# Optimization experiments

Measured on AMD Instinct MI355X. Metric: run time of the kernel, lower is better.

The kernel has to match this reference:

```python
import jax, jax.numpy as jnp
import numpy as np

N = 100000
IN_CH = 1024
Z = 32
E = 1600000


def _gcn_conv(x, src, dst, W, b, n_nodes):
    # PyG GCNConv: add self-loops, symmetric deg^{-1/2} normalization,
    # message = norm * (x @ W)[src], scatter-add into dst, plus bias.
    loop = jnp.arange(n_nodes)
    s = jnp.concatenate([src, loop])
    d = jnp.concatenate([dst, loop])
    deg = jax.ops.segment_sum(jnp.ones_like(s, dtype=x.dtype), d, num_segments=n_nodes)
    dinv = jnp.where(deg > 0, jax.lax.rsqrt(deg), 0.0)
    norm = dinv[s] * dinv[d]                     # [E+N]
    h = x @ W                                    # [N, out]
    msg = h[s] * norm[:, None]                   # [E+N, out]
    out = jax.ops.segment_sum(msg, d, num_segments=n_nodes)
    return out + b


def setup_inputs() -> dict:
    key = jax.random.key(0)
    ks = jax.random.split(key, 10)
    x = jax.random.normal(ks[0], (N, IN_CH), dtype=jnp.float32)
    edge_index = jax.random.randint(ks[1], (2, E), 0, N, dtype=jnp.int64)
    def lin(k, fan_in, fan_out):
        bound = 1.0 / np.sqrt(fan_in)
        kw, kb = jax.random.split(k)
        W = jax.random.uniform(kw, (fan_in, fan_out), jnp.float32, -bound, bound)
        b = jax.random.uniform(kb, (fan_out,), jnp.float32, -bound, bound)
        return W, b
    Wg1, bg1 = lin(ks[2], IN_CH, 2 * Z)
    Wg2, bg2 = lin(ks[3], 2 * Z, Z)
    Wf1, bf1 = lin(ks[4], Z, 2 * Z)
    Wf2, bf2 = lin(ks[5], 2 * Z, IN_CH)
    return {"x": x, "edge_index": edge_index,
            "Wg1": Wg1, "bg1": bg1, "Wg2": Wg2, "bg2": bg2,
            "Wf1": Wf1, "bf1": bf1, "Wf2": Wf2, "bf2": bf2}


def reference(x, edge_index, Wg1, bg1, Wg2, bg2, Wf1, bf1, Wf2, bf2):
    src, dst = edge_index[0], edge_index[1]
    h = jax.nn.relu(_gcn_conv(x, src, dst, Wg1, bg1, N))
    z = _gcn_conv(h, src, dst, Wg2, bg2, N)          # encode output
    d = jax.nn.relu(z @ Wf1 + bf1)
    out = jax.nn.relu(d @ Wf2 + bf2)                 # decode output
    return out
```

## Files before the change

### kernel.cpp

```cpp
#include <hip/hip_runtime.h>

#define NN 100000
#define EE 1600000

using bf16x8 = __attribute__((ext_vector_type(8))) short;
using f32x4  = __attribute__((ext_vector_type(4))) float;

static __device__ __forceinline__ unsigned short f2bh(float f) {
    unsigned int u = __float_as_uint(f);
    return (unsigned short)((u + 0x7FFFu + ((u >> 16) & 1u)) >> 16);
}
static __device__ __forceinline__ float bh2f(unsigned short h) {
    return __uint_as_float(((unsigned int)h) << 16);
}

static __device__ __forceinline__ void split_pack(float4 a, float4 b,
                                                  bf16x8& h, bf16x8& l) {
    float f[8] = {a.x, a.y, a.z, a.w, b.x, b.y, b.z, b.w};
    union { bf16x8 v; unsigned int u[4]; } H, L;
    #pragma unroll
    for (int e = 0; e < 4; ++e) {
        unsigned int u0 = __float_as_uint(f[2 * e]);
        unsigned int u1 = __float_as_uint(f[2 * e + 1]);
        H.u[e] = (u0 >> 16) | (u1 & 0xFFFF0000u);
        float r0 = f[2 * e]     - __uint_as_float(u0 & 0xFFFF0000u);
        float r1 = f[2 * e + 1] - __uint_as_float(u1 & 0xFFFF0000u);
        L.u[e] = (__float_as_uint(r0) >> 16) | (__float_as_uint(r1) & 0xFFFF0000u);
    }
    h = H.v; l = L.v;
}

__global__ __launch_bounds__(256) void k_init(unsigned int* cursor) {
    int v = blockIdx.x * 256 + threadIdx.x;
    if (v < NN) cursor[v] = 0u;
}

__global__ __launch_bounds__(256) void k_fill(const int* __restrict__ src,
        const int* __restrict__ dst, unsigned int* cursor, int* __restrict__ bkt) {
    int e = blockIdx.x * 256 + threadIdx.x;
    if (e < EE) {
        int d = dst[e];
        unsigned int pos = atomicAdd(&cursor[d], 1u);
        bkt[(size_t)d * 64 + pos] = src[e];
    }
}

__global__ __launch_bounds__(256) void k_dinv(const unsigned int* __restrict__ deg, float* dinv) {
    int v = blockIdx.x * 256 + threadIdx.x;
    if (v < NN) dinv[v] = rsqrtf((float)(deg[v] + 1u));
}

__global__ __launch_bounds__(256) void k_prepW1(const float* __restrict__ W,
        unsigned short* __restrict__ img) {
    int t = blockIdx.x * 256 + threadIdx.x;
    int k = t >> 6, c = t & 63;
    float f = W[k * 64 + c];
    unsigned short h = f2bh(f);
    int chunk = k >> 5, kk = k & 31;
    size_t base = (size_t)chunk * 4608 + (size_t)c * 36 + kk;
    img[base] = h;
    img[base + 2304] = f2bh(f - bh2f(h));
}

__global__ __launch_bounds__(256) void k_prepW2(const float* __restrict__ W,
        unsigned short* __restrict__ wh, unsigned short* __restrict__ wl) {
    int t = blockIdx.x * 256 + threadIdx.x;
    int k = t >> 10, c = t & 1023;
    float f = W[k * 1024 + c];
    unsigned short h = f2bh(f);
    wh[c * 64 + k] = h;
    wl[c * 64 + k] = f2bh(f - bh2f(h));
}

__global__ __launch_bounds__(256) void k_gemm1(const float* __restrict__ x,
        const unsigned short* __restrict__ wimg,
        const float* __restrict__ dinv, float* __restrict__ g1) {
    __shared__ __align__(16) unsigned short bs[2][2][64][36];
    const int tid = threadIdx.x;
    const int lane = tid & 63, w = tid >> 6;
    const int l16 = lane & 15, g = lane >> 4;
    const int row0 = blockIdx.x * 64;
    const int rA = row0 + w * 16 + l16;
    const bool okA = rA < NN;
    const float* xp = x + (size_t)rA * 1024 + g * 8;
    const char* wb = (const char*)wimg;
    f32x4 acc[4] = {};
    for (int j = w; j < 9; j += 4)
        __builtin_amdgcn_global_load_lds((const unsigned int*)(wb + j * 1024 + lane * 16),
                                         (unsigned int*)((char*)&bs[0][0][0][0] + j * 1024), 16, 0, 0);
    float4 xr0 = make_float4(0.f,0.f,0.f,0.f), xr1 = xr0;
    if (okA) { xr0 = *(const float4*)(xp); xr1 = *(const float4*)(xp + 4); }
    __syncthreads();
    int cur = 0;
    for (int t = 0; t < 32; ++t) {
        float4 nx0 = make_float4(0.f,0.f,0.f,0.f), nx1 = nx0;
        if (t < 31) {
            const char* gb = wb + (size_t)(t + 1) * 9216;
            char* lb = (char*)&bs[cur ^ 1][0][0][0];
            for (int j = w; j < 9; j += 4)
                __builtin_amdgcn_global_load_lds((const unsigned int*)(gb + j * 1024 + lane * 16),
                                                 (unsigned int*)(lb + j * 1024), 16, 0, 0);
            if (okA) { nx0 = *(const float4*)(xp + (t + 1) * 32);
                       nx1 = *(const float4*)(xp + (t + 1) * 32 + 4); }
        }
        bf16x8 ah, al;
        split_pack(xr0, xr1, ah, al);
        #pragma unroll
        for (int nf = 0; nf < 4; ++nf) {
            bf16x8 bh = *(const bf16x8*)&bs[cur][0][nf * 16 + l16][g * 8];
            bf16x8 bl = *(const bf16x8*)&bs[cur][1][nf * 16 + l16][g * 8];
            acc[nf] = __builtin_amdgcn_mfma_f32_16x16x32_bf16(ah, bh, acc[nf], 0, 0, 0);
            acc[nf] = __builtin_amdgcn_mfma_f32_16x16x32_bf16(al, bh, acc[nf], 0, 0, 0);
            acc[nf] = __builtin_amdgcn_mfma_f32_16x16x32_bf16(ah, bl, acc[nf], 0, 0, 0);
        }
        __syncthreads();
        xr0 = nx0; xr1 = nx1; cur ^= 1;
    }
    #pragma unroll
    for (int r = 0; r < 4; ++r) {
        int node = row0 + w * 16 + g * 4 + r;
        if (node < NN) {
            float di = dinv[node];
            #pragma unroll
            for (int nf = 0; nf < 4; ++nf)
                g1[(size_t)node * 64 + nf * 16 + l16] = acc[nf][r] * di;
        }
    }
}

__global__ __launch_bounds__(256) void k_gather64(const float* __restrict__ g1,
        const int* __restrict__ bkt, const unsigned int* __restrict__ deg,
        const float* __restrict__ dinv, const float* __restrict__ bg1,
        float* __restrict__ h) {
    int wv = (blockIdx.x * 256 + threadIdx.x) >> 6;
    int lane = threadIdx.x & 63;
    if (wv >= NN) return;
    unsigned int n = deg[wv];
    const int* b = bkt + (size_t)wv * 64;
    float sum = g1[(size_t)wv * 64 + lane];
    unsigned int i = 0;
    for (; i + 4 <= n; i += 4) {
        int s0 = b[i], s1 = b[i + 1], s2 = b[i + 2], s3 = b[i + 3];
        float v0 = g1[(size_t)s0 * 64 + lane];
        float v1 = g1[(size_t)s1 * 64 + lane];
        float v2 = g1[(size_t)s2 * 64 + lane];
        float v3 = g1[(size_t)s3 * 64 + lane];
        sum += (v0 + v1) + (v2 + v3);
    }
    for (; i < n; ++i) sum += g1[(size_t)b[i] * 64 + lane];
    h[(size_t)wv * 64 + lane] = fmaxf(sum * dinv[wv] + bg1[lane], 0.f);
}

__global__ __launch_bounds__(256) void k_layer2(const float* __restrict__ h,
        const float* __restrict__ Wg2, const float* __restrict__ dinv,
        float* __restrict__ g2) {
    __shared__ __align__(16) float as[64][68];
    __shared__ __align__(16) float wsh[64][32];
    const int tid = threadIdx.x;
    const int node0 = blockIdx.x * 64;
    {
        const int lr = tid >> 4, lk = (tid & 15) * 4;
        #pragma unroll
        for (int l = 0; l < 4; ++l) {
            int r = lr + l * 16, v = node0 + r;
            float4 a = make_float4(0.f, 0.f, 0.f, 0.f);
            if (v < NN) a = *(const float4*)(h + (size_t)v * 64 + lk);
            *(float4*)&as[r][lk] = a;
        }
        const int wr = tid >> 3, wk = (tid & 7) * 4;
        #pragma unroll
        for (int l = 0; l < 2; ++l) {
            int r = wr + l * 32;
            *(float4*)&wsh[r][wk] = *(const float4*)(Wg2 + (size_t)r * 32 + wk);
        }
    }
    __syncthreads();
    const int tx = tid & 7, ty = tid >> 3;
    float acc[2][4] = {{0.f}};
    for (int kk = 0; kk < 64; kk += 4) {
        float wv[4][4];
        #pragma unroll
        for (int j = 0; j < 4; ++j)
            *(float4*)&wv[j][0] = *(const float4*)&wsh[kk + j][tx * 4];
        #pragma unroll
        for (int i = 0; i < 2; ++i) {
            float xv[4];
            *(float4*)&xv[0] = *(const float4*)&as[ty * 2 + i][kk];
            #pragma unroll
            for (int j = 0; j < 4; ++j) {
                #pragma unroll
                for (int c = 0; c < 4; ++c)
                    acc[i][c] += xv[j] * wv[j][c];
            }
        }
    }
    #pragma unroll
    for (int i = 0; i < 2; ++i) {
        int v = node0 + ty * 2 + i;
        if (v < NN) {
            float di = dinv[v];
            float4 o;
            o.x = acc[i][0] * di; o.y = acc[i][1] * di;
            o.z = acc[i][2] * di; o.w = acc[i][3] * di;
            *(float4*)(g2 + (size_t)v * 32 + tx * 4) = o;
        }
    }
}

__global__ __launch_bounds__(256) void k_gather32(const float* __restrict__ g2,
        const int* __restrict__ bkt, const unsigned int* __restrict__ deg,
        const float* __restrict__ dinv, const float* __restrict__ bg2,
        float* __restrict__ z) {
    int node = (blockIdx.x * 256 + threadIdx.x) >> 5;
    int c = threadIdx.x & 31;
    if (node >= NN) return;
    unsigned int n = deg[node];
    const int* b = bkt + (size_t)node * 64;
    float sum = g2[(size_t)node * 32 + c];
    unsigned int i = 0;
    for (; i + 4 <= n; i += 4) {
        int s0 = b[i], s1 = b[i + 1], s2 = b[i + 2], s3 = b[i + 3];
        float v0 = g2[(size_t)s0 * 32 + c];
        float v1 = g2[(size_t)s1 * 32 + c];
        float v2 = g2[(size_t)s2 * 32 + c];
        float v3 = g2[(size_t)s3 * 32 + c];
        sum += (v0 + v1) + (v2 + v3);
    }
    for (; i < n; ++i) sum += g2[(size_t)b[i] * 32 + c];
    z[(size_t)node * 32 + c] = sum * dinv[node] + bg2[c];
}

__global__ __launch_bounds__(256) void k_decode(const float* __restrict__ z,
        const float* __restrict__ Wf1, const float* __restrict__ bf1,
        const unsigned short* __restrict__ w2hg, const unsigned short* __restrict__ w2lg,
        const float* __restrict__ bf2, float* __restrict__ out) {
    __shared__ __align__(16) unsigned char smem[35328];
    float (*dsh)[68] = (float (*)[68])smem;
    float (*zs)[36]  = (float (*)[36])(smem + 17408);
    float (*w1s)[64] = (float (*)[64])(smem + 26624);
    unsigned short (*w2h)[72] = (unsigned short (*)[72])smem;
    unsigned short (*w2l)[72] = (unsigned short (*)[72])(smem + 9216);
    float (*ost)[66] = (float (*)[66])(smem + 18432);
    const int tid = threadIdx.x;
    const int lane = tid & 63, w = tid >> 6;
    const int l16 = lane & 15, g = lane >> 4;
    const int node0 = blockIdx.x * 64;

    uint4 ph[2], pl[2];
    #pragma unroll
    for (int j = 0; j < 2; ++j) {
        int fi = tid + 256 * j;
        int c = fi >> 3, k8 = (fi & 7) * 8;
        ph[j] = *(const uint4*)(w2hg + (size_t)c * 64 + k8);
        pl[j] = *(const uint4*)(w2lg + (size_t)c * 64 + k8);
    }

    #pragma unroll
    for (int j = 0; j < 2; ++j) {
        int fi = tid + 256 * j;
        int v = fi >> 3, m4 = (fi & 7) * 4;
        float4 zz = make_float4(0.f, 0.f, 0.f, 0.f);
        if (node0 + v < NN) zz = *(const float4*)(z + (size_t)(node0 + v) * 32 + m4);
        *(float4*)&zs[v][m4] = zz;
    }
    #pragma unroll
    for (int j = 0; j < 2; ++j) {
        int fi = tid + 256 * j;
        int r = fi >> 4, c4 = (fi & 15) * 4;
        *(float4*)&w1s[r][c4] = *(const float4*)(Wf1 + (size_t)r * 64 + c4);
    }
    __syncthreads();

    {
        const int dtx = tid & 15, dty = tid >> 4;
        float acc[4][4] = {{0.f}};
        for (int m = 0; m < 32; m += 4) {
            float wv[4][4];
            #pragma unroll
            for (int j = 0; j < 4; ++j)
                *(float4*)&wv[j][0] = *(const float4*)&w1s[m + j][dtx * 4];
            #pragma unroll
            for (int i = 0; i < 4; ++i) {
                float zv[4];
                *(float4*)&zv[0] = *(const float4*)&zs[dty * 4 + i][m];
                #pragma unroll
                for (int j = 0; j < 4; ++j) {
                    #pragma unroll
                    for (int c = 0; c < 4; ++c)
                        acc[i][c] += zv[j] * wv[j][c];
                }
            }
        }
        float4 b4 = *(const float4*)(bf1 + dtx * 4);
        #pragma unroll
        for (int i = 0; i < 4; ++i) {
            float4 dd;
            dd.x = fmaxf(acc[i][0] + b4.x, 0.f);
            dd.y = fmaxf(acc[i][1] + b4.y, 0.f);
            dd.z = fmaxf(acc[i][2] + b4.z, 0.f);
            dd.w = fmaxf(acc[i][3] + b4.w, 0.f);
            *(float4*)&dsh[dty * 4 + i][dtx * 4] = dd;
        }
    }
    __syncthreads();

    bf16x8 ah[2], al[2];
    {
        int row = w * 16 + l16;
        #pragma unroll
        for (int s = 0; s < 2; ++s) {
            int k0 = s * 32 + g * 8;
            float4 f0 = *(float4*)&dsh[row][k0];
            float4 f1 = *(float4*)&dsh[row][k0 + 4];
            float fv[8] = {f0.x, f0.y, f0.z, f0.w, f1.x, f1.y, f1.z, f1.w};
            bf16x8 hv, lv;
            #pragma unroll
            for (int e = 0; e < 8; ++e) {
                unsigned short hh = f2bh(fv[e]);
                hv[e] = (short)hh;
                lv[e] = (short)f2bh(fv[e] - bh2f(hh));
            }
            ah[s] = hv; al[s] = lv;
        }
    }
    __syncthreads();

    #pragma unroll
    for (int j = 0; j < 2; ++j) {
        int fi = tid + 256 * j;
        int c = fi >> 3, k8 = (fi & 7) * 8;
        *(uint4*)&w2h[c][k8] = ph[j];
        *(uint4*)&w2l[c][k8] = pl[j];
        ph[j] = *(const uint4*)(w2hg + (size_t)(64 + c) * 64 + k8);
        pl[j] = *(const uint4*)(w2lg + (size_t)(64 + c) * 64 + k8);
    }
    __syncthreads();

    for (int ch = 0; ch < 16; ++ch) {
        const int col0 = ch * 64;
        f32x4 acc[4] = {};
        #pragma unroll
        for (int nf = 0; nf < 4; ++nf) {
            int c = nf * 16 + l16;
            #pragma unroll
            for (int s = 0; s < 2; ++s) {
                int k0 = s * 32 + g * 8;
                bf16x8 bh = *(const bf16x8*)&w2h[c][k0];
                bf16x8 bl = *(const bf16x8*)&w2l[c][k0];
                acc[nf] = __builtin_amdgcn_mfma_f32_16x16x32_bf16(ah[s], bh, acc[nf], 0, 0, 0);
                acc[nf] = __builtin_amdgcn_mfma_f32_16x16x32_bf16(al[s], bh, acc[nf], 0, 0, 0);
                acc[nf] = __builtin_amdgcn_mfma_f32_16x16x32_bf16(ah[s], bl, acc[nf], 0, 0, 0);
            }
        }
        #pragma unroll
        for (int nf = 0; nf < 4; ++nf) {
            float b = bf2[col0 + nf * 16 + l16];
            #pragma unroll
            for (int r = 0; r < 4; ++r)
                ost[w * 16 + g * 4 + r][nf * 16 + l16] = fmaxf(acc[nf][r] + b, 0.f);
        }
        __syncthreads();
        if (ch < 15) {
            #pragma unroll
            for (int j = 0; j < 2; ++j) {
                int fi = tid + 256 * j;
                int c = fi >> 3, k8 = (fi & 7) * 8;
                *(uint4*)&w2h[c][k8] = ph[j];
                *(uint4*)&w2l[c][k8] = pl[j];
                if (ch < 14) {
                    ph[j] = *(const uint4*)(w2hg + (size_t)((ch + 2) * 64 + c) * 64 + k8);
                    pl[j] = *(const uint4*)(w2lg + (size_t)((ch + 2) * 64 + c) * 64 + k8);
                }
            }
        }
        #pragma unroll
        for (int j = 0; j < 4; ++j) {
            int fi = tid + 256 * j;
            int row = fi >> 4, c4 = (fi & 15) * 4;
            int node = node0 + row;
            if (node < NN) {
                float4 o = *(float4*)&ost[row][c4];
                *(float4*)(out + (size_t)node * 1024 + col0 + c4) = o;
            }
        }
        __syncthreads();
    }
}

extern "C" void kernel_launch(void* const* d_in, const int* in_sizes, int n_in,
                              void* d_out, int out_size, void* d_ws, size_t ws_size,
                              hipStream_t stream) {
    const float* x   = (const float*)d_in[0];
    const int* ei    = (const int*)d_in[1];
    const float* Wg1 = (const float*)d_in[2];
    const float* bg1 = (const float*)d_in[3];
    const float* Wg2 = (const float*)d_in[4];
    const float* bg2 = (const float*)d_in[5];
    const float* Wf1 = (const float*)d_in[6];
    const float* bf1 = (const float*)d_in[7];
    const float* Wf2 = (const float*)d_in[8];
    const float* bf2 = (const float*)d_in[9];
    float* out = (float*)d_out;
    float* ws  = (float*)d_ws;

    const int* src = ei;
    const int* dst = ei + EE;

    float* dinv = ws;
    float* g2   = ws + NN;
    float* z    = ws + NN + 32 * NN;
    unsigned short* wf2h = (unsigned short*)g2;
    unsigned short* wf2l = wf2h + 64 * 1024;

    float* g1 = out;
    float* h  = out + (size_t)64 * NN;
    int* bkt  = (int*)(out + (size_t)128 * NN);
    unsigned int* cursor = (unsigned int*)(bkt + (size_t)64 * NN);
    unsigned short* wg1img = (unsigned short*)(cursor + NN);

    k_init  <<<(NN + 255) / 256, 256, 0, stream>>>(cursor);
    k_fill  <<<(EE + 255) / 256, 256, 0, stream>>>(src, dst, cursor, bkt);
    k_dinv  <<<(NN + 255) / 256, 256, 0, stream>>>(cursor, dinv);
    k_prepW1<<<256, 256, 0, stream>>>(Wg1, wg1img);
    k_gemm1 <<<(NN + 63) / 64, 256, 0, stream>>>(x, wg1img, dinv, g1);
    k_gather64<<<(NN * 64 + 255) / 256, 256, 0, stream>>>(g1, bkt, cursor, dinv, bg1, h);
    k_layer2<<<(NN + 63) / 64, 256, 0, stream>>>(h, Wg2, dinv, g2);
    k_gather32<<<(NN * 32 + 255) / 256, 256, 0, stream>>>(g2, bkt, cursor, dinv, bg2, z);
    k_prepW2<<<256, 256, 0, stream>>>(Wf2, wf2h, wf2l);
    k_decode<<<(NN + 63) / 64, 256, 0, stream>>>(z, Wf1, bf1, wf2h, wf2l, bf2, out);
}
```

Measured before the change: 609.1 us.

## Retile GEMM1 to 128 rows with triple-buffered K=64 stages; sort edge buckets

The first-layer GEMM now gives each block 128 rows and works in K steps of 64. It uses a three-stage LDS ring with explicit vmcnt waits and raw barriers, so each weight tile in LDS is reused across twice as many rows and the barrier count falls. The W1 prep and cursor init are merged into one kernel. A new bitonic sort orders each node's neighbour bucket, which makes the gathers deterministic and more local. The sort adds a launch and a pass over the buckets, and the hand-tuned vmcnt counts are fragile.

```diff
diff --git a/kernel.cpp b/kernel.cpp
--- a/kernel.cpp
+++ b/kernel.cpp
@@ -30,9 +30,20 @@
     h = H.v; l = L.v;
 }
 
-__global__ __launch_bounds__(256) void k_init(unsigned int* cursor) {
-    int v = blockIdx.x * 256 + threadIdx.x;
-    if (v < NN) cursor[v] = 0u;
+__global__ __launch_bounds__(256) void k_prep(const float* __restrict__ Wg1,
+        unsigned short* __restrict__ img, unsigned int* __restrict__ cursor) {
+    int t = blockIdx.x * 256 + threadIdx.x;
+    if (t < 65536) {
+        int k = t >> 6, c = t & 63;
+        float f = Wg1[t];
+        unsigned short hh = f2bh(f);
+        int chunk = k >> 6, kk = k & 63;
+        size_t base = (size_t)chunk * 9216 + (size_t)c * 72 + kk;
+        img[base] = hh;
+        img[base + 4608] = f2bh(f - bh2f(hh));
+    } else if (t < 65536 + NN) {
+        cursor[t - 65536] = 0u;
+    }
 }
 
 __global__ __launch_bounds__(256) void k_fill(const int* __restrict__ src,
@@ -45,21 +56,28 @@
     }
 }
 
+__global__ __launch_bounds__(256) void k_sort(int* __restrict__ bkt,
+        const unsigned int* __restrict__ deg) {
+    int v = (blockIdx.x * 256 + threadIdx.x) >> 6;
+    int lane = threadIdx.x & 63;
+    if (v >= NN) return;
+    int n = (int)deg[v];
+    int val = (lane < n) ? bkt[(size_t)v * 64 + lane] : 0x7FFFFFFF;
+    #pragma unroll
+    for (int k = 2; k <= 64; k <<= 1) {
+        #pragma unroll
+        for (int j = k >> 1; j > 0; j >>= 1) {
+            int partner = __shfl_xor(val, j, 64);
+            bool takeMin = (((lane & k) == 0) == ((lane & j) == 0));
+            val = takeMin ? min(val, partner) : max(val, partner);
+        }
+    }
+    if (lane < n) bkt[(size_t)v * 64 + lane] = val;
+}
+
 __global__ __launch_bounds__(256) void k_dinv(const unsigned int* __restrict__ deg, float* dinv) {
     int v = blockIdx.x * 256 + threadIdx.x;
     if (v < NN) dinv[v] = rsqrtf((float)(deg[v] + 1u));
-}
-
-__global__ __launch_bounds__(256) void k_prepW1(const float* __restrict__ W,
-        unsigned short* __restrict__ img) {
-    int t = blockIdx.x * 256 + threadIdx.x;
-    int k = t >> 6, c = t & 63;
-    float f = W[k * 64 + c];
-    unsigned short h = f2bh(f);
-    int chunk = k >> 5, kk = k & 31;
-    size_t base = (size_t)chunk * 4608 + (size_t)c * 36 + kk;
-    img[base] = h;
-    img[base + 2304] = f2bh(f - bh2f(h));
 }
 
 __global__ __launch_bounds__(256) void k_prepW2(const float* __restrict__ W,
@@ -75,55 +93,88 @@
 __global__ __launch_bounds__(256) void k_gemm1(const float* __restrict__ x,
         const unsigned short* __restrict__ wimg,
         const float* __restrict__ dinv, float* __restrict__ g1) {
-    __shared__ __align__(16) unsigned short bs[2][2][64][36];
+    __shared__ __align__(16) unsigned short bs[3][2][64][72];
     const int tid = threadIdx.x;
     const int lane = tid & 63, w = tid >> 6;
     const int l16 = lane & 15, g = lane >> 4;
-    const int row0 = blockIdx.x * 64;
-    const int rA = row0 + w * 16 + l16;
-    const bool okA = rA < NN;
-    const float* xp = x + (size_t)rA * 1024 + g * 8;
-    const char* wb = (const char*)wimg;
-    f32x4 acc[4] = {};
-    for (int j = w; j < 9; j += 4)
-        __builtin_amdgcn_global_load_lds((const unsigned int*)(wb + j * 1024 + lane * 16),
-                                         (unsigned int*)((char*)&bs[0][0][0][0] + j * 1024), 16, 0, 0);
-    float4 xr0 = make_float4(0.f,0.f,0.f,0.f), xr1 = xr0;
-    if (okA) { xr0 = *(const float4*)(xp); xr1 = *(const float4*)(xp + 4); }
-    __syncthreads();
-    int cur = 0;
-    for (int t = 0; t < 32; ++t) {
-        float4 nx0 = make_float4(0.f,0.f,0.f,0.f), nx1 = nx0;
-        if (t < 31) {
-            const char* gb = wb + (size_t)(t + 1) * 9216;
-            char* lb = (char*)&bs[cur ^ 1][0][0][0];
-            for (int j = w; j < 9; j += 4)
-                __builtin_amdgcn_global_load_lds((const unsigned int*)(gb + j * 1024 + lane * 16),
-                                                 (unsigned int*)(lb + j * 1024), 16, 0, 0);
-            if (okA) { nx0 = *(const float4*)(xp + (t + 1) * 32);
-                       nx1 = *(const float4*)(xp + (t + 1) * 32 + 4); }
-        }
-        bf16x8 ah, al;
-        split_pack(xr0, xr1, ah, al);
-        #pragma unroll
-        for (int nf = 0; nf < 4; ++nf) {
-            bf16x8 bh = *(const bf16x8*)&bs[cur][0][nf * 16 + l16][g * 8];
-            bf16x8 bl = *(const bf16x8*)&bs[cur][1][nf * 16 + l16][g * 8];
-            acc[nf] = __builtin_amdgcn_mfma_f32_16x16x32_bf16(ah, bh, acc[nf], 0, 0, 0);
-            acc[nf] = __builtin_amdgcn_mfma_f32_16x16x32_bf16(al, bh, acc[nf], 0, 0, 0);
-            acc[nf] = __builtin_amdgcn_mfma_f32_16x16x32_bf16(ah, bl, acc[nf], 0, 0, 0);
-        }
-        __syncthreads();
-        xr0 = nx0; xr1 = nx1; cur ^= 1;
-    }
-    #pragma unroll
-    for (int r = 0; r < 4; ++r) {
-        int node = row0 + w * 16 + g * 4 + r;
-        if (node < NN) {
-            float di = dinv[node];
-            #pragma unroll
-            for (int nf = 0; nf < 4; ++nf)
-                g1[(size_t)node * 64 + nf * 16 + l16] = acc[nf][r] * di;
+    const int row0 = blockIdx.x * 128 + w * 16;
+    const int rA0 = row0 + l16, rA1 = row0 + 64 + l16;
+    const bool ok0 = rA0 < NN, ok1 = rA1 < NN;
+    const float* xp0 = x + (size_t)rA0 * 1024 + g * 8;
+    const float* xp1 = x + (size_t)rA1 * 1024 + g * 8;
+    const float4 f40 = make_float4(0.f, 0.f, 0.f, 0.f);
+    f32x4 acc[2][4] = {};
+
+    auto stage = [&](int t) {
+        const char* gb = (const char*)wimg + (size_t)t * 18432;
+        char* lb = (char*)&bs[t % 3][0][0][0];
+        for (int j = w; j < 18; j += 4)
+            __builtin_amdgcn_global_load_lds((const unsigned int*)(gb + j * 1024 + lane * 16),
+                                             (unsigned int*)(lb + j * 1024), 16, 0, 0);
+    };
+    auto xload = [&](int t, float4 xv[8]) {
+        const int k0 = t * 64;
+        #pragma unroll
+        for (int s = 0; s < 2; ++s) {
+            xv[s * 2 + 0]     = ok0 ? *(const float4*)(xp0 + k0 + s * 32)     : f40;
+            xv[s * 2 + 1]     = ok0 ? *(const float4*)(xp0 + k0 + s * 32 + 4) : f40;
+            xv[4 + s * 2 + 0] = ok1 ? *(const float4*)(xp1 + k0 + s * 32)     : f40;
+            xv[4 + s * 2 + 1] = ok1 ? *(const float4*)(xp1 + k0 + s * 32 + 4) : f40;
+        }
+    };
+    auto compute = [&](int t, float4 xv[8]) {
+        const int b = t % 3;
+        #pragma unroll
+        for (int s = 0; s < 2; ++s) {
+            bf16x8 ah0, al0, ah1, al1;
+            split_pack(xv[s * 2], xv[s * 2 + 1], ah0, al0);
+            split_pack(xv[4 + s * 2], xv[4 + s * 2 + 1], ah1, al1);
+            #pragma unroll
+            for (int nf = 0; nf < 4; ++nf) {
+                bf16x8 bh = *(const bf16x8*)&bs[b][0][nf * 16 + l16][s * 32 + g * 8];
+                bf16x8 bl = *(const bf16x8*)&bs[b][1][nf * 16 + l16][s * 32 + g * 8];
+                acc[0][nf] = __builtin_amdgcn_mfma_f32_16x16x32_bf16(ah0, bh, acc[0][nf], 0, 0, 0);
+                acc[1][nf] = __builtin_amdgcn_mfma_f32_16x16x32_bf16(ah1, bh, acc[1][nf], 0, 0, 0);
+                acc[0][nf] = __builtin_amdgcn_mfma_f32_16x16x32_bf16(al0, bh, acc[0][nf], 0, 0, 0);
+                acc[1][nf] = __builtin_amdgcn_mfma_f32_16x16x32_bf16(al1, bh, acc[1][nf], 0, 0, 0);
+                acc[0][nf] = __builtin_amdgcn_mfma_f32_16x16x32_bf16(ah0, bl, acc[0][nf], 0, 0, 0);
+                acc[1][nf] = __builtin_amdgcn_mfma_f32_16x16x32_bf16(ah1, bl, acc[1][nf], 0, 0, 0);
+            }
+        }
+    };
+
+    float4 xA[8], xB[8];
+    stage(0); stage(1);
+    xload(0, xA);
+    if (w < 2) asm volatile("s_waitcnt vmcnt(5)" ::: "memory");
+    else       asm volatile("s_waitcnt vmcnt(4)" ::: "memory");
+    __builtin_amdgcn_s_barrier();
+
+    for (int t = 0; t < 16; ++t) {
+        if (t + 2 < 16) stage(t + 2);
+        if (t + 1 < 16) { if (t & 1) xload(t + 1, xA); else xload(t + 1, xB); }
+        if (t & 1) compute(t, xB); else compute(t, xA);
+        if (t + 1 < 16) {
+            if (t + 2 < 16) {
+                if (w < 2) asm volatile("s_waitcnt vmcnt(13)" ::: "memory");
+                else       asm volatile("s_waitcnt vmcnt(12)" ::: "memory");
+            } else {
+                asm volatile("s_waitcnt vmcnt(8)" ::: "memory");
+            }
+            __builtin_amdgcn_s_barrier();
+        }
+    }
+    #pragma unroll
+    for (int mf = 0; mf < 2; ++mf) {
+        #pragma unroll
+        for (int r = 0; r < 4; ++r) {
+            int node = row0 + mf * 64 + g * 4 + r;
+            if (node < NN) {
+                float di = dinv[node];
+                #pragma unroll
+                for (int nf = 0; nf < 4; ++nf)
+                    g1[(size_t)node * 64 + nf * 16 + l16] = acc[mf][nf][r] * di;
+            }
         }
     }
 }
@@ -418,11 +469,11 @@
     unsigned int* cursor = (unsigned int*)(bkt + (size_t)64 * NN);
     unsigned short* wg1img = (unsigned short*)(cursor + NN);
 
-    k_init  <<<(NN + 255) / 256, 256, 0, stream>>>(cursor);
+    k_prep  <<<(65536 + NN + 255) / 256, 256, 0, stream>>>(Wg1, wg1img, cursor);
     k_fill  <<<(EE + 255) / 256, 256, 0, stream>>>(src, dst, cursor, bkt);
+    k_sort  <<<(NN * 64 + 255) / 256, 256, 0, stream>>>(bkt, cursor);
     k_dinv  <<<(NN + 255) / 256, 256, 0, stream>>>(cursor, dinv);
-    k_prepW1<<<256, 256, 0, stream>>>(Wg1, wg1img);
-    k_gemm1 <<<(NN + 63) / 64, 256, 0, stream>>>(x, wg1img, dinv, g1);
+    k_gemm1 <<<(NN + 127) / 128, 256, 0, stream>>>(x, wg1img, dinv, g1);
     k_gather64<<<(NN * 64 + 255) / 256, 256, 0, stream>>>(g1, bkt, cursor, dinv, bg1, h);
     k_layer2<<<(NN + 63) / 64, 256, 0, stream>>>(h, Wg2, dinv, g2);
     k_gather32<<<(NN * 32 + 255) / 256, 256, 0, stream>>>(g2, bkt, cursor, dinv, bg2, z);
```

Result: slower. 742.2 us (+21.8%).

## Fuse weight prep and cursor init, bitonic-sort per-node neighbor buckets

Applied to the files above, without the earlier changes.

Merges the cursor zeroing and both weight-splitting prep kernels into one launch, and moves Wf2's bf16 image to its own workspace region so it can be prepared up front. Adds a per-node wavefront bitonic sort of the bucketed source indices, which also computes dinv. Sorting makes the gather order deterministic and gives more locality when reading neighbor rows. The cost is an extra pass that reads and writes the full bucket array.

```diff
diff --git a/kernel.cpp b/kernel.cpp
--- a/kernel.cpp
+++ b/kernel.cpp
@@ -30,9 +30,30 @@
     h = H.v; l = L.v;
 }
 
-__global__ __launch_bounds__(256) void k_init(unsigned int* cursor) {
-    int v = blockIdx.x * 256 + threadIdx.x;
-    if (v < NN) cursor[v] = 0u;
+__global__ __launch_bounds__(256) void k_prep(const float* __restrict__ Wg1,
+        const float* __restrict__ Wf2,
+        unsigned short* __restrict__ w1img,
+        unsigned short* __restrict__ w2h, unsigned short* __restrict__ w2l,
+        unsigned int* __restrict__ cursor) {
+    int t = blockIdx.x * 256 + threadIdx.x;
+    if (t < 65536) {
+        int k = t >> 6, c = t & 63;
+        float f = Wg1[t];
+        unsigned short hh = f2bh(f);
+        int chunk = k >> 5, kk = k & 31;
+        size_t base = (size_t)chunk * 4608 + (size_t)c * 36 + kk;
+        w1img[base] = hh;
+        w1img[base + 2304] = f2bh(f - bh2f(hh));
+    } else if (t < 131072) {
+        int tt = t - 65536;
+        int k = tt >> 10, c = tt & 1023;
+        float f = Wf2[tt];
+        unsigned short hh = f2bh(f);
+        w2h[c * 64 + k] = hh;
+        w2l[c * 64 + k] = f2bh(f - bh2f(hh));
+    } else if (t < 131072 + NN) {
+        cursor[t - 131072] = 0u;
+    }
 }
 
 __global__ __launch_bounds__(256) void k_fill(const int* __restrict__ src,
@@ -45,31 +66,24 @@
     }
 }
 
-__global__ __launch_bounds__(256) void k_dinv(const unsigned int* __restrict__ deg, float* dinv) {
-    int v = blockIdx.x * 256 + threadIdx.x;
-    if (v < NN) dinv[v] = rsqrtf((float)(deg[v] + 1u));
-}
-
-__global__ __launch_bounds__(256) void k_prepW1(const float* __restrict__ W,
-        unsigned short* __restrict__ img) {
-    int t = blockIdx.x * 256 + threadIdx.x;
-    int k = t >> 6, c = t & 63;
-    float f = W[k * 64 + c];
-    unsigned short h = f2bh(f);
-    int chunk = k >> 5, kk = k & 31;
-    size_t base = (size_t)chunk * 4608 + (size_t)c * 36 + kk;
-    img[base] = h;
-    img[base + 2304] = f2bh(f - bh2f(h));
-}
-
-__global__ __launch_bounds__(256) void k_prepW2(const float* __restrict__ W,
-        unsigned short* __restrict__ wh, unsigned short* __restrict__ wl) {
-    int t = blockIdx.x * 256 + threadIdx.x;
-    int k = t >> 10, c = t & 1023;
-    float f = W[k * 1024 + c];
-    unsigned short h = f2bh(f);
-    wh[c * 64 + k] = h;
-    wl[c * 64 + k] = f2bh(f - bh2f(h));
+__global__ __launch_bounds__(256) void k_sort(int* __restrict__ bkt,
+        const unsigned int* __restrict__ deg, float* __restrict__ dinv) {
+    int v = (blockIdx.x * 256 + threadIdx.x) >> 6;
+    int lane = threadIdx.x & 63;
+    if (v >= NN) return;
+    int n = (int)deg[v];
+    if (lane == 0) dinv[v] = rsqrtf((float)(n + 1));
+    int val = (lane < n) ? bkt[(size_t)v * 64 + lane] : 0x7FFFFFFF;
+    #pragma unroll
+    for (int k = 2; k <= 64; k <<= 1) {
+        #pragma unroll
+        for (int j = k >> 1; j > 0; j >>= 1) {
+            int partner = __shfl_xor(val, j, 64);
+            bool takeMin = (((lane & k) == 0) == ((lane & j) == 0));
+            val = takeMin ? min(val, partner) : max(val, partner);
+        }
+    }
+    if (lane < n) bkt[(size_t)v * 64 + lane] = val;
 }
 
 __global__ __launch_bounds__(256) void k_gemm1(const float* __restrict__ x,
@@ -409,7 +423,7 @@
     float* dinv = ws;
     float* g2   = ws + NN;
     float* z    = ws + NN + 32 * NN;
-    unsigned short* wf2h = (unsigned short*)g2;
+    unsigned short* wf2h = (unsigned short*)(ws + NN + 64 * NN);
     unsigned short* wf2l = wf2h + 64 * 1024;
 
     float* g1 = out;
@@ -418,14 +432,12 @@
     unsigned int* cursor = (unsigned int*)(bkt + (size_t)64 * NN);
     unsigned short* wg1img = (unsigned short*)(cursor + NN);
 
-    k_init  <<<(NN + 255) / 256, 256, 0, stream>>>(cursor);
+    k_prep  <<<(131072 + NN + 255) / 256, 256, 0, stream>>>(Wg1, Wf2, wg1img, wf2h, wf2l, cursor);
     k_fill  <<<(EE + 255) / 256, 256, 0, stream>>>(src, dst, cursor, bkt);
-    k_dinv  <<<(NN + 255) / 256, 256, 0, stream>>>(cursor, dinv);
-    k_prepW1<<<256, 256, 0, stream>>>(Wg1, wg1img);
+    k_sort  <<<(NN * 64 + 255) / 256, 256, 0, stream>>>(bkt, cursor, dinv);
     k_gemm1 <<<(NN + 63) / 64, 256, 0, stream>>>(x, wg1img, dinv, g1);
     k_gather64<<<(NN * 64 + 255) / 256, 256, 0, stream>>>(g1, bkt, cursor, dinv, bg1, h);
     k_layer2<<<(NN + 63) / 64, 256, 0, stream>>>(h, Wg2, dinv, g2);
     k_gather32<<<(NN * 32 + 255) / 256, 256, 0, stream>>>(g2, bkt, cursor, dinv, bg2, z);
-    k_prepW2<<<256, 256, 0, stream>>>(Wf2, wf2h, wf2l);
     k_decode<<<(NN + 63) / 64, 256, 0, stream>>>(z, Wf1, bf1, wf2h, wf2l, bf2, out);
 }
```

After: 651.4 us. 6.9% more time.
